# Kernel optimization log

Hardware: AMD Instinct MI355X
Metric: run time of the kernel (lower is better)

Reference implementation:

```python
import jax, jax.numpy as jnp
import numpy as np

D_MODEL = 1024
NUM_HEADS = 16
D_K = D_MODEL // NUM_HEADS
B, T = 2, 2048


def setup_inputs() -> dict:
    key = jax.random.key(0)
    ks = jax.random.split(key, 9)
    s = 1.0 / np.sqrt(D_MODEL)
    inp = {"x": jax.random.normal(ks[0], (B, T, D_MODEL), dtype=jnp.float32)}
    for i, name in enumerate(["q", "k", "v", "out"]):
        inp[f"W_{name}"] = jax.random.uniform(ks[1 + 2 * i], (D_MODEL, D_MODEL), jnp.float32, -s, s)
        inp[f"b_{name}"] = jax.random.uniform(ks[2 + 2 * i], (D_MODEL,), jnp.float32, -s, s)
    return inp


def reference(x, W_q, b_q, W_k, b_k, W_v, b_v, W_out, b_out):
    b, t, _ = x.shape
    # torch Linear: y = x @ W.T + b
    def proj(inp, W, bias):
        y = inp @ W.T + bias
        return y.reshape(b, -1, NUM_HEADS, D_K).transpose(0, 2, 1, 3)  # [B,H,T,d_k]

    Q = proj(x, W_q, b_q)
    K = proj(x, W_k, b_k)
    V = proj(x, W_v, b_v)
    scores = jnp.einsum("bhqd,bhkd->bhqk", Q, K) / jnp.sqrt(jnp.float32(D_K))
    attn = jax.nn.softmax(scores, axis=-1)
    ctx = jnp.einsum("bhqk,bhkd->bhqd", attn, V)
    ctx = ctx.transpose(0, 2, 1, 3).reshape(b, t, D_MODEL)
    return ctx @ W_out.T + b_out
```

## Files before the change

### kernel.cpp

```cpp
#include <hip/hip_runtime.h>
#include <hip/hip_bf16.h>

typedef __attribute__((ext_vector_type(8))) short short8;
typedef __attribute__((ext_vector_type(4))) short short4v;
typedef __attribute__((ext_vector_type(4))) float floatx4;

__device__ __forceinline__ unsigned short f2b(float f) {
  unsigned int v;
  __builtin_memcpy(&v, &f, 4);
  unsigned int r = (v + 0x7FFFu + ((v >> 16) & 1u)) >> 16;
  return (unsigned short)r;
}

__device__ __forceinline__ void async_copy16(const void* g, void* l) {
  __builtin_amdgcn_global_load_lds(
      (const __attribute__((address_space(1))) unsigned int*)g,
      (__attribute__((address_space(3))) unsigned int*)l, 16, 0, 0);
}

__global__ __launch_bounds__(256) void cvt_all_kernel(
    const float* __restrict__ x,
    const float* __restrict__ w0, const float* __restrict__ w1,
    const float* __restrict__ w2, const float* __restrict__ w3,
    unsigned short* __restrict__ xb,
    unsigned short* __restrict__ d0, unsigned short* __restrict__ d1,
    unsigned short* __restrict__ d2, unsigned short* __restrict__ d3)
{
  int gid = blockIdx.x * 256 + threadIdx.x;
  const float* src;
  unsigned short* dst;
  size_t off;
  if (gid < (1 << 20)) {
    src = x; dst = xb; off = gid;
  } else {
    int g = gid - (1 << 20);
    int w = g >> 18;
    off = g & 0x3FFFF;
    src = (w == 0) ? w0 : (w == 1) ? w1 : (w == 2) ? w2 : w3;
    dst = (w == 0) ? d0 : (w == 1) ? d1 : (w == 2) ? d2 : d3;
  }
  floatx4 v = *(const floatx4*)(src + off * 4);
  alignas(8) unsigned short r[4];
#pragma unroll
  for (int j = 0; j < 4; ++j) r[j] = f2b(v[j]);
  *(unsigned long long*)(dst + off * 4) = *(const unsigned long long*)r;
}

template <bool F32OUT>
__global__ __launch_bounds__(256) void gemm_bias_kernel(
    const unsigned short* __restrict__ A,
    const unsigned short* __restrict__ W0, const unsigned short* __restrict__ W1,
    const unsigned short* __restrict__ W2,
    const float* __restrict__ bias0, const float* __restrict__ bias1,
    const float* __restrict__ bias2,
    unsigned short* __restrict__ D0, unsigned short* __restrict__ D1,
    unsigned short* __restrict__ D2, float* __restrict__ DF)
{
  const int z = blockIdx.z;
  const unsigned short* W  = (z == 0) ? W0 : (z == 1) ? W1 : W2;
  const float* bias        = (z == 0) ? bias0 : (z == 1) ? bias1 : bias2;
  unsigned short* Dst      = (z == 0) ? D0 : (z == 1) ? D1 : D2;

  __shared__ alignas(16) unsigned short sA[128 * 32];
  __shared__ alignas(16) unsigned short sB[128 * 32];

  const int tid  = threadIdx.x;
  const int lane = tid & 63;
  const int wave = tid >> 6;
  const int col  = lane & 15;
  const int quad = lane >> 4;
  const int wm   = (wave >> 1) * 64;
  const int wn   = (wave & 1) * 64;
  const int m0   = blockIdx.y * 128;
  const int n0   = blockIdx.x * 128;

  floatx4 acc[4][4];
#pragma unroll
  for (int i = 0; i < 4; ++i)
#pragma unroll
    for (int j = 0; j < 4; ++j) acc[i][j] = (floatx4){0.f, 0.f, 0.f, 0.f};

  for (int k0 = 0; k0 < 1024; k0 += 32) {
    __syncthreads();
#pragma unroll
    for (int i = 0; i < 2; ++i) {
      int c   = i * 256 + tid;
      int row = c >> 2;
      int ko  = (c & 3) * 8;
      async_copy16(A + (size_t)(m0 + row) * 1024 + k0 + ko, sA + c * 8);
      async_copy16(W + (size_t)(n0 + row) * 1024 + k0 + ko, sB + c * 8);
    }
    __syncthreads();
    short8 af[4], bf[4];
#pragma unroll
    for (int mi = 0; mi < 4; ++mi)
      af[mi] = *(const short8*)(sA + (wm + mi * 16 + col) * 32 + quad * 8);
#pragma unroll
    for (int ni = 0; ni < 4; ++ni)
      bf[ni] = *(const short8*)(sB + (wn + ni * 16 + col) * 32 + quad * 8);
#pragma unroll
    for (int mi = 0; mi < 4; ++mi)
#pragma unroll
      for (int ni = 0; ni < 4; ++ni)
        acc[mi][ni] = __builtin_amdgcn_mfma_f32_16x16x32_bf16(af[mi], bf[ni], acc[mi][ni], 0, 0, 0);
  }

#pragma unroll
  for (int ni = 0; ni < 4; ++ni) {
    int n = n0 + wn + ni * 16 + col;
    float bv = bias[n];
#pragma unroll
    for (int mi = 0; mi < 4; ++mi) {
      int mbase = m0 + wm + mi * 16 + quad * 4;
#pragma unroll
      for (int r = 0; r < 4; ++r) {
        float val = acc[mi][ni][r] + bv;
        if (F32OUT) DF[(size_t)(mbase + r) * 1024 + n] = val;
        else        Dst[(size_t)(mbase + r) * 1024 + n] = f2b(val);
      }
    }
  }
}

__global__ __launch_bounds__(256) void transpose_v_kernel(
    const unsigned short* __restrict__ V, unsigned short* __restrict__ VT)
{
  __shared__ alignas(16) unsigned short tile[64][72];
  const int bh = blockIdx.x;
  const int b = bh >> 4, h = bh & 15;
  const int t0 = blockIdx.y * 64;
  const int tid = threadIdx.x;

#pragma unroll
  for (int i = 0; i < 2; ++i) {
    int c = i * 256 + tid;
    int tr = c >> 3;
    int doff = (c & 7) * 8;
    short8 v = *(const short8*)(V + (size_t)(b * 2048 + t0 + tr) * 1024 + h * 64 + doff);
    *(short8*)(&tile[tr][doff]) = v;
  }
  __syncthreads();
#pragma unroll
  for (int i = 0; i < 2; ++i) {
    int c = i * 256 + tid;
    int d = c >> 3;
    int toff = (c & 7) * 8;
    alignas(16) unsigned short tmp[8];
#pragma unroll
    for (int j = 0; j < 8; ++j) tmp[j] = tile[toff + j][d];
    *(short8*)(VT + ((size_t)bh * 64 + d) * 2048 + t0 + toff) = *(const short8*)tmp;
  }
}

__global__ __launch_bounds__(256) void attention_kernel(
    const unsigned short* __restrict__ Q, const unsigned short* __restrict__ K,
    const unsigned short* __restrict__ VT, unsigned short* __restrict__ CTX)
{
  __shared__ alignas(16) unsigned short sQ[2 * 64 * 32];
  __shared__ alignas(16) unsigned short sK[2 * 64 * 32];
  __shared__ alignas(16) unsigned short sV[2 * 64 * 32];
  __shared__ alignas(16) unsigned short sP[4][2 * 16 * 36];

  const int bh = blockIdx.x;
  const int b = bh >> 4, h = bh & 15;
  const int q0 = blockIdx.y * 64;
  const int tid  = threadIdx.x;
  const int lane = tid & 63;
  const int wave = tid >> 6;
  const int col  = lane & 15;
  const int quad = lane >> 4;

#pragma unroll
  for (int i = 0; i < 2; ++i) {
    int r = tid >> 2;
    int ko = (tid & 3) * 8;
    async_copy16(Q + (size_t)(b * 2048 + q0 + r) * 1024 + h * 64 + i * 32 + ko,
                 sQ + (i * 256 + tid) * 8);
  }
  __syncthreads();
  short8 qf[2];
  qf[0] = *(const short8*)(sQ + (wave * 16 + col) * 32 + quad * 8);
  qf[1] = *(const short8*)(sQ + 2048 + (wave * 16 + col) * 32 + quad * 8);

  floatx4 Oacc[4];
#pragma unroll
  for (int f = 0; f < 4; ++f) Oacc[f] = (floatx4){0.f, 0.f, 0.f, 0.f};
  float lacc[4] = {0.f, 0.f, 0.f, 0.f};
  const float scale = 0.125f;

  unsigned short* myP = &sP[wave][0];

  for (int kt = 0; kt < 2048; kt += 64) {
    __syncthreads();
#pragma unroll
    for (int i = 0; i < 2; ++i) {
      int r = tid >> 2;
      int ko = (tid & 3) * 8;
      async_copy16(K + (size_t)(b * 2048 + kt + r) * 1024 + h * 64 + i * 32 + ko,
                   sK + (i * 256 + tid) * 8);
      async_copy16(VT + ((size_t)bh * 64 + r) * 2048 + kt + i * 32 + ko,
                   sV + (i * 256 + tid) * 8);
    }
    __syncthreads();

    floatx4 S[4];
#pragma unroll
    for (int f = 0; f < 4; ++f) {
      S[f] = (floatx4){0.f, 0.f, 0.f, 0.f};
      short8 kf0 = *(const short8*)(sK + (f * 16 + col) * 32 + quad * 8);
      S[f] = __builtin_amdgcn_mfma_f32_16x16x32_bf16(qf[0], kf0, S[f], 0, 0, 0);
      short8 kf1 = *(const short8*)(sK + 2048 + (f * 16 + col) * 32 + quad * 8);
      S[f] = __builtin_amdgcn_mfma_f32_16x16x32_bf16(qf[1], kf1, S[f], 0, 0, 0);
    }

#pragma unroll
    for (int f = 0; f < 4; ++f) {
      int base = (f >> 1) * 576 + (f & 1) * 16 + col;
#pragma unroll
      for (int r = 0; r < 4; ++r) {
        float p = __expf(S[f][r] * scale);
        lacc[r] += p;
        myP[base + (quad * 4 + r) * 36] = f2b(p);
      }
    }

    short8 pf0, pf1;
    {
      const unsigned short* p0 = myP + col * 36 + quad * 8;
      short4v lo = *(const short4v*)p0;
      short4v hi = *(const short4v*)(p0 + 4);
      pf0 = (short8){lo[0], lo[1], lo[2], lo[3], hi[0], hi[1], hi[2], hi[3]};
      const unsigned short* p1 = p0 + 576;
      short4v lo1 = *(const short4v*)p1;
      short4v hi1 = *(const short4v*)(p1 + 4);
      pf1 = (short8){lo1[0], lo1[1], lo1[2], lo1[3], hi1[0], hi1[1], hi1[2], hi1[3]};
    }
#pragma unroll
    for (int f = 0; f < 4; ++f) {
      short8 vf0 = *(const short8*)(sV + (f * 16 + col) * 32 + quad * 8);
      Oacc[f] = __builtin_amdgcn_mfma_f32_16x16x32_bf16(pf0, vf0, Oacc[f], 0, 0, 0);
      short8 vf1 = *(const short8*)(sV + 2048 + (f * 16 + col) * 32 + quad * 8);
      Oacc[f] = __builtin_amdgcn_mfma_f32_16x16x32_bf16(pf1, vf1, Oacc[f], 0, 0, 0);
    }
  }

#pragma unroll
  for (int s = 1; s < 16; s <<= 1) {
#pragma unroll
    for (int r = 0; r < 4; ++r) lacc[r] += __shfl_xor(lacc[r], s, 64);
  }

#pragma unroll
  for (int f = 0; f < 4; ++f) {
#pragma unroll
    for (int r = 0; r < 4; ++r) {
      int q = q0 + wave * 16 + quad * 4 + r;
      int d = f * 16 + col;
      CTX[(size_t)(b * 2048 + q) * 1024 + h * 64 + d] = f2b(Oacc[f][r] / lacc[r]);
    }
  }
}

extern "C" void kernel_launch(void* const* d_in, const int* in_sizes, int n_in,
                              void* d_out, int out_size, void* d_ws, size_t ws_size,
                              hipStream_t stream) {
  const float* x   = (const float*)d_in[0];
  const float* W_q = (const float*)d_in[1];
  const float* b_q = (const float*)d_in[2];
  const float* W_k = (const float*)d_in[3];
  const float* b_k = (const float*)d_in[4];
  const float* W_v = (const float*)d_in[5];
  const float* b_v = (const float*)d_in[6];
  const float* W_o = (const float*)d_in[7];
  const float* b_o = (const float*)d_in[8];
  float* out = (float*)d_out;

  const size_t NX = (size_t)4096 * 1024;
  const size_t NW = (size_t)1024 * 1024;

  unsigned short* p   = (unsigned short*)d_ws;
  unsigned short* xb  = p;  p += NX;
  unsigned short* Wqb = p;  p += NW;
  unsigned short* Wkb = p;  p += NW;
  unsigned short* Wvb = p;  p += NW;
  unsigned short* Wob = p;  p += NW;
  unsigned short* Q   = p;  p += NX;
  unsigned short* Kb  = p;  p += NX;
  unsigned short* V   = p;  p += NX;
  unsigned short* VT  = p;  p += NX;
  unsigned short* CTX = V;

  dim3 blk(256);
  cvt_all_kernel<<<dim3(8192), blk, 0, stream>>>(
      x, W_q, W_k, W_v, W_o, xb, Wqb, Wkb, Wvb, Wob);

  gemm_bias_kernel<false><<<dim3(8, 32, 3), blk, 0, stream>>>(
      xb, Wqb, Wkb, Wvb, b_q, b_k, b_v, Q, Kb, V, nullptr);
  transpose_v_kernel<<<dim3(32, 32), blk, 0, stream>>>(V, VT);
  attention_kernel<<<dim3(32, 32), blk, 0, stream>>>(Q, Kb, VT, CTX);
  gemm_bias_kernel<true><<<dim3(8, 32, 1), blk, 0, stream>>>(
      CTX, Wob, Wob, Wob, b_o, b_o, b_o, nullptr, nullptr, nullptr, out);
}
```

Baseline: 221.8 us.

## Fuse V transpose into QKV GEMM, fold softmax scale, and retile output GEMM

The QKV GEMM epilogue now writes V directly in transposed layout, which removes the separate transpose kernel and one intermediate buffer. Q is pre-scaled by log2(e)/sqrt(d_k), so attention can use exp2 directly. Attention computes S transposed, packing P into LDS with a single 64-bit store per fragment and fewer reads, and reduces the row sum with fewer shuffles. The output projection gets its own kernel with 128x64 tiles, giving more blocks, and conversions use packed bf16 instructions. The transposed V stores are strided, scattered 2-byte writes, which may cost more than the removed kernel.

```diff
diff --git a/kernel.cpp b/kernel.cpp
--- a/kernel.cpp
+++ b/kernel.cpp
@@ -2,7 +2,6 @@
 #include <hip/hip_bf16.h>
 
 typedef __attribute__((ext_vector_type(8))) short short8;
-typedef __attribute__((ext_vector_type(4))) short short4v;
 typedef __attribute__((ext_vector_type(4))) float floatx4;
 
 __device__ __forceinline__ unsigned short f2b(float f) {
@@ -12,11 +11,33 @@
   return (unsigned short)r;
 }
 
+__device__ __forceinline__ unsigned int f2b_pk(float a, float b) {
+#if __has_builtin(__builtin_amdgcn_cvt_pk_bf16_f32)
+  typedef __attribute__((ext_vector_type(2))) __bf16 bf16x2;
+  bf16x2 r = __builtin_amdgcn_cvt_pk_bf16_f32(a, b);
+  unsigned int u;
+  __builtin_memcpy(&u, &r, 4);
+  return u;
+#else
+  return ((unsigned int)f2b(b) << 16) | (unsigned int)f2b(a);
+#endif
+}
+
+__device__ __forceinline__ float fast_exp2(float x) {
+#if __has_builtin(__builtin_amdgcn_exp2f)
+  return __builtin_amdgcn_exp2f(x);
+#else
+  return __builtin_exp2f(x);
+#endif
+}
+
 __device__ __forceinline__ void async_copy16(const void* g, void* l) {
   __builtin_amdgcn_global_load_lds(
       (const __attribute__((address_space(1))) unsigned int*)g,
       (__attribute__((address_space(3))) unsigned int*)l, 16, 0, 0);
 }
+
+#define QSCALE 0.18033688011112042f
 
 __global__ __launch_bounds__(256) void cvt_all_kernel(
     const float* __restrict__ x,
@@ -40,26 +61,23 @@
     dst = (w == 0) ? d0 : (w == 1) ? d1 : (w == 2) ? d2 : d3;
   }
   floatx4 v = *(const floatx4*)(src + off * 4);
-  alignas(8) unsigned short r[4];
-#pragma unroll
-  for (int j = 0; j < 4; ++j) r[j] = f2b(v[j]);
-  *(unsigned long long*)(dst + off * 4) = *(const unsigned long long*)r;
-}
-
-template <bool F32OUT>
-__global__ __launch_bounds__(256) void gemm_bias_kernel(
+  unsigned int lo = f2b_pk(v[0], v[1]), hi = f2b_pk(v[2], v[3]);
+  unsigned long long r = ((unsigned long long)hi << 32) | lo;
+  *(unsigned long long*)(dst + off * 4) = r;
+}
+
+__global__ __launch_bounds__(256) void gemm_qkv_kernel(
     const unsigned short* __restrict__ A,
     const unsigned short* __restrict__ W0, const unsigned short* __restrict__ W1,
     const unsigned short* __restrict__ W2,
     const float* __restrict__ bias0, const float* __restrict__ bias1,
     const float* __restrict__ bias2,
-    unsigned short* __restrict__ D0, unsigned short* __restrict__ D1,
-    unsigned short* __restrict__ D2, float* __restrict__ DF)
+    unsigned short* __restrict__ Qo, unsigned short* __restrict__ Ko,
+    unsigned short* __restrict__ VTo)
 {
   const int z = blockIdx.z;
   const unsigned short* W  = (z == 0) ? W0 : (z == 1) ? W1 : W2;
   const float* bias        = (z == 0) ? bias0 : (z == 1) ? bias1 : bias2;
-  unsigned short* Dst      = (z == 0) ? D0 : (z == 1) ? D1 : D2;
 
   __shared__ alignas(16) unsigned short sA[128 * 32];
   __shared__ alignas(16) unsigned short sB[128 * 32];
@@ -114,41 +132,85 @@
       int mbase = m0 + wm + mi * 16 + quad * 4;
 #pragma unroll
       for (int r = 0; r < 4; ++r) {
+        int m = mbase + r;
         float val = acc[mi][ni][r] + bv;
-        if (F32OUT) DF[(size_t)(mbase + r) * 1024 + n] = val;
-        else        Dst[(size_t)(mbase + r) * 1024 + n] = f2b(val);
+        if (z == 0) {
+          Qo[(size_t)m * 1024 + n] = f2b(val * QSCALE);
+        } else if (z == 1) {
+          Ko[(size_t)m * 1024 + n] = f2b(val);
+        } else {
+          int d = n & 63, h = n >> 6;
+          int bb = m >> 11, t = m & 2047;
+          VTo[(((size_t)bb * 16 + h) * 64 + d) * 2048 + t] = f2b(val);
+        }
       }
     }
   }
 }
 
-__global__ __launch_bounds__(256) void transpose_v_kernel(
-    const unsigned short* __restrict__ V, unsigned short* __restrict__ VT)
+__global__ __launch_bounds__(256) void gemm_out_kernel(
+    const unsigned short* __restrict__ A, const unsigned short* __restrict__ W,
+    const float* __restrict__ bias, float* __restrict__ DF)
 {
-  __shared__ alignas(16) unsigned short tile[64][72];
-  const int bh = blockIdx.x;
-  const int b = bh >> 4, h = bh & 15;
-  const int t0 = blockIdx.y * 64;
-  const int tid = threadIdx.x;
-
-#pragma unroll
-  for (int i = 0; i < 2; ++i) {
-    int c = i * 256 + tid;
-    int tr = c >> 3;
-    int doff = (c & 7) * 8;
-    short8 v = *(const short8*)(V + (size_t)(b * 2048 + t0 + tr) * 1024 + h * 64 + doff);
-    *(short8*)(&tile[tr][doff]) = v;
-  }
-  __syncthreads();
-#pragma unroll
-  for (int i = 0; i < 2; ++i) {
-    int c = i * 256 + tid;
-    int d = c >> 3;
-    int toff = (c & 7) * 8;
-    alignas(16) unsigned short tmp[8];
-#pragma unroll
-    for (int j = 0; j < 8; ++j) tmp[j] = tile[toff + j][d];
-    *(short8*)(VT + ((size_t)bh * 64 + d) * 2048 + t0 + toff) = *(const short8*)tmp;
+  __shared__ alignas(16) unsigned short sA[128 * 32];
+  __shared__ alignas(16) unsigned short sB[64 * 32];
+
+  const int tid  = threadIdx.x;
+  const int lane = tid & 63;
+  const int wave = tid >> 6;
+  const int col  = lane & 15;
+  const int quad = lane >> 4;
+  const int wm   = (wave >> 1) * 64;
+  const int wn   = (wave & 1) * 32;
+  const int m0   = blockIdx.y * 128;
+  const int n0   = blockIdx.x * 64;
+
+  floatx4 acc[4][2];
+#pragma unroll
+  for (int i = 0; i < 4; ++i)
+#pragma unroll
+    for (int j = 0; j < 2; ++j) acc[i][j] = (floatx4){0.f, 0.f, 0.f, 0.f};
+
+  for (int k0 = 0; k0 < 1024; k0 += 32) {
+    __syncthreads();
+#pragma unroll
+    for (int i = 0; i < 2; ++i) {
+      int c   = i * 256 + tid;
+      int row = c >> 2;
+      int ko  = (c & 3) * 8;
+      async_copy16(A + (size_t)(m0 + row) * 1024 + k0 + ko, sA + c * 8);
+    }
+    {
+      int row = tid >> 2;
+      int ko  = (tid & 3) * 8;
+      async_copy16(W + (size_t)(n0 + row) * 1024 + k0 + ko, sB + tid * 8);
+    }
+    __syncthreads();
+    short8 af[4], bf[2];
+#pragma unroll
+    for (int mi = 0; mi < 4; ++mi)
+      af[mi] = *(const short8*)(sA + (wm + mi * 16 + col) * 32 + quad * 8);
+#pragma unroll
+    for (int ni = 0; ni < 2; ++ni)
+      bf[ni] = *(const short8*)(sB + (wn + ni * 16 + col) * 32 + quad * 8);
+#pragma unroll
+    for (int mi = 0; mi < 4; ++mi)
+#pragma unroll
+      for (int ni = 0; ni < 2; ++ni)
+        acc[mi][ni] = __builtin_amdgcn_mfma_f32_16x16x32_bf16(af[mi], bf[ni], acc[mi][ni], 0, 0, 0);
+  }
+
+#pragma unroll
+  for (int ni = 0; ni < 2; ++ni) {
+    int n = n0 + wn + ni * 16 + col;
+    float bv = bias[n];
+#pragma unroll
+    for (int mi = 0; mi < 4; ++mi) {
+      int mbase = m0 + wm + mi * 16 + quad * 4;
+#pragma unroll
+      for (int r = 0; r < 4; ++r)
+        DF[(size_t)(mbase + r) * 1024 + n] = acc[mi][ni][r] + bv;
+    }
   }
 }
 
@@ -159,7 +221,7 @@
   __shared__ alignas(16) unsigned short sQ[2 * 64 * 32];
   __shared__ alignas(16) unsigned short sK[2 * 64 * 32];
   __shared__ alignas(16) unsigned short sV[2 * 64 * 32];
-  __shared__ alignas(16) unsigned short sP[4][2 * 16 * 36];
+  __shared__ alignas(16) unsigned short sP[4][16 * 72];
 
   const int bh = blockIdx.x;
   const int b = bh >> 4, h = bh & 15;
@@ -185,8 +247,7 @@
   floatx4 Oacc[4];
 #pragma unroll
   for (int f = 0; f < 4; ++f) Oacc[f] = (floatx4){0.f, 0.f, 0.f, 0.f};
-  float lacc[4] = {0.f, 0.f, 0.f, 0.f};
-  const float scale = 0.125f;
+  float lacc = 0.f;
 
   unsigned short* myP = &sP[wave][0];
 
@@ -203,38 +264,30 @@
     }
     __syncthreads();
 
-    floatx4 S[4];
+    floatx4 ST[4];
 #pragma unroll
     for (int f = 0; f < 4; ++f) {
-      S[f] = (floatx4){0.f, 0.f, 0.f, 0.f};
+      ST[f] = (floatx4){0.f, 0.f, 0.f, 0.f};
       short8 kf0 = *(const short8*)(sK + (f * 16 + col) * 32 + quad * 8);
-      S[f] = __builtin_amdgcn_mfma_f32_16x16x32_bf16(qf[0], kf0, S[f], 0, 0, 0);
+      ST[f] = __builtin_amdgcn_mfma_f32_16x16x32_bf16(kf0, qf[0], ST[f], 0, 0, 0);
       short8 kf1 = *(const short8*)(sK + 2048 + (f * 16 + col) * 32 + quad * 8);
-      S[f] = __builtin_amdgcn_mfma_f32_16x16x32_bf16(qf[1], kf1, S[f], 0, 0, 0);
+      ST[f] = __builtin_amdgcn_mfma_f32_16x16x32_bf16(kf1, qf[1], ST[f], 0, 0, 0);
     }
 
 #pragma unroll
     for (int f = 0; f < 4; ++f) {
-      int base = (f >> 1) * 576 + (f & 1) * 16 + col;
-#pragma unroll
-      for (int r = 0; r < 4; ++r) {
-        float p = __expf(S[f][r] * scale);
-        lacc[r] += p;
-        myP[base + (quad * 4 + r) * 36] = f2b(p);
-      }
-    }
-
-    short8 pf0, pf1;
-    {
-      const unsigned short* p0 = myP + col * 36 + quad * 8;
-      short4v lo = *(const short4v*)p0;
-      short4v hi = *(const short4v*)(p0 + 4);
-      pf0 = (short8){lo[0], lo[1], lo[2], lo[3], hi[0], hi[1], hi[2], hi[3]};
-      const unsigned short* p1 = p0 + 576;
-      short4v lo1 = *(const short4v*)p1;
-      short4v hi1 = *(const short4v*)(p1 + 4);
-      pf1 = (short8){lo1[0], lo1[1], lo1[2], lo1[3], hi1[0], hi1[1], hi1[2], hi1[3]};
-    }
+      float p0 = fast_exp2(ST[f][0]);
+      float p1 = fast_exp2(ST[f][1]);
+      float p2 = fast_exp2(ST[f][2]);
+      float p3 = fast_exp2(ST[f][3]);
+      lacc += (p0 + p1) + (p2 + p3);
+      unsigned long long w =
+          ((unsigned long long)f2b_pk(p2, p3) << 32) | f2b_pk(p0, p1);
+      *(unsigned long long*)(myP + col * 72 + f * 16 + quad * 4) = w;
+    }
+
+    short8 pf0 = *(const short8*)(myP + col * 72 + quad * 8);
+    short8 pf1 = *(const short8*)(myP + col * 72 + 32 + quad * 8);
 #pragma unroll
     for (int f = 0; f < 4; ++f) {
       short8 vf0 = *(const short8*)(sV + (f * 16 + col) * 32 + quad * 8);
@@ -244,11 +297,11 @@
     }
   }
 
-#pragma unroll
-  for (int s = 1; s < 16; s <<= 1) {
-#pragma unroll
-    for (int r = 0; r < 4; ++r) lacc[r] += __shfl_xor(lacc[r], s, 64);
-  }
+  lacc += __shfl_xor(lacc, 16, 64);
+  lacc += __shfl_xor(lacc, 32, 64);
+  float inv[4];
+#pragma unroll
+  for (int r = 0; r < 4; ++r) inv[r] = 1.f / __shfl(lacc, quad * 4 + r, 16);
 
 #pragma unroll
   for (int f = 0; f < 4; ++f) {
@@ -256,7 +309,7 @@
     for (int r = 0; r < 4; ++r) {
       int q = q0 + wave * 16 + quad * 4 + r;
       int d = f * 16 + col;
-      CTX[(size_t)(b * 2048 + q) * 1024 + h * 64 + d] = f2b(Oacc[f][r] / lacc[r]);
+      CTX[(size_t)(b * 2048 + q) * 1024 + h * 64 + d] = f2b(Oacc[f][r] * inv[r]);
     }
   }
 }
@@ -286,18 +339,14 @@
   unsigned short* Wob = p;  p += NW;
   unsigned short* Q   = p;  p += NX;
   unsigned short* Kb  = p;  p += NX;
-  unsigned short* V   = p;  p += NX;
   unsigned short* VT  = p;  p += NX;
-  unsigned short* CTX = V;
+  unsigned short* CTX = p;  p += NX;
 
   dim3 blk(256);
   cvt_all_kernel<<<dim3(8192), blk, 0, stream>>>(
       x, W_q, W_k, W_v, W_o, xb, Wqb, Wkb, Wvb, Wob);
-
-  gemm_bias_kernel<false><<<dim3(8, 32, 3), blk, 0, stream>>>(
-      xb, Wqb, Wkb, Wvb, b_q, b_k, b_v, Q, Kb, V, nullptr);
-  transpose_v_kernel<<<dim3(32, 32), blk, 0, stream>>>(V, VT);
+  gemm_qkv_kernel<<<dim3(8, 32, 3), blk, 0, stream>>>(
+      xb, Wqb, Wkb, Wvb, b_q, b_k, b_v, Q, Kb, VT);
   attention_kernel<<<dim3(32, 32), blk, 0, stream>>>(Q, Kb, VT, CTX);
-  gemm_bias_kernel<true><<<dim3(8, 32, 1), blk, 0, stream>>>(
-      CTX, Wob, Wob, Wob, b_o, b_o, b_o, nullptr, nullptr, nullptr, out);
-}
+  gemm_out_kernel<<<dim3(16, 32), blk, 0, stream>>>(CTX, Wob, b_o, out);
+}
```

Result: faster. 215.8 us (-2.7%).
